# Kernel optimization log

Hardware: AMD Instinct MI355X
Metric: run time of the kernel (lower is better)

The kernel has to match this reference:

```python
import jax, jax.numpy as jnp
import numpy as np

B, C, H, W = 1, 96, 128, 128
P = 4            # patch_size
E = 192          # embed_dim
DI = 384         # d_inner = expand * embed_dim
NS = 16          # d_state
R = 12           # dt_rank = ceil(E/16)
K = 4            # scan directions
NBLK = 8         # SS2D_MBs_num
GW = C // 2      # SCPA group width


def layernorm(x, g, b, eps=1e-5):
    mu = x.mean(-1, keepdims=True)
    v = x.var(-1, keepdims=True)
    return (x - mu) * jax.lax.rsqrt(v + eps) * g + b


def batchnorm(x, g, b, m, v, eps=1e-5):
    # eval-mode BatchNorm2d over channel axis 1 of (B,C,H,W)
    return (x - m[:, None, None]) * jax.lax.rsqrt(v + eps)[:, None, None] * g[:, None, None] + b[:, None, None]


def conv2d(x, w):
    return jax.lax.conv_general_dilated(x, w, (1, 1), 'SAME', dimension_numbers=('NCHW', 'OIHW', 'NCHW'))


def dwconv2d(x, w, b):
    out = jax.lax.conv_general_dilated(x, w[:, None], (1, 1), 'SAME',
                                       dimension_numbers=('NCHW', 'OIHW', 'NCHW'),
                                       feature_group_count=w.shape[0])
    return out + b[None, :, None, None]


def lrelu(x):
    return jnp.where(x >= 0, x, 0.2 * x)


def channel_attention(x, w1, w2):
    # CBAM-style: shared MLP on avg+max pooled channel descriptors, sigmoid gate
    avg = x.mean((2, 3))
    mx = x.max((2, 3))
    mlp = lambda v: jax.nn.relu(v @ w1.T) @ w2.T
    attn = jax.nn.sigmoid(mlp(avg) + mlp(mx))
    return x * attn[:, :, None, None]


def selective_scan(xs, dts, A, Bs, Cs, Dskip):
    # xs,dts: (B,K,DI,L); A: (K,DI,NS); Bs,Cs: (B,K,NS,L); Dskip: (K,DI)
    xs_t = jnp.moveaxis(xs, -1, 0)
    dts_t = jnp.moveaxis(dts, -1, 0)
    Bs_t = jnp.moveaxis(Bs, -1, 0)
    Cs_t = jnp.moveaxis(Cs, -1, 0)
    h0 = jnp.zeros(xs.shape[:3] + (NS,), xs.dtype)  # (B,K,DI,NS)

    def step(h, t):
        xt, dt, Bt, Ct = t
        h = jnp.exp(dt[..., None] * A) * h + (dt * xt)[..., None] * Bt[:, :, None, :]
        return h, jnp.sum(h * Ct[:, :, None, :], axis=-1)

    _, ys = jax.lax.scan(step, h0, (xs_t, dts_t, Bs_t, Cs_t))
    return jnp.moveaxis(ys, 0, -1) + xs * Dskip[None, :, :, None]


def ss2d_block(x, p):
    # VMamba-style VSS block: x + SS2D(LN(x)); x: (B,Hp,Wp,E)
    (ln_g, ln_b, inproj_w, conv_w, conv_b, xproj_w, dtproj_w, dtproj_b,
     Alog, Dskip, on_g, on_b, outproj_w, merge_w) = p
    Bsz, Hp, Wp, _ = x.shape
    L = Hp * Wp
    h = layernorm(x, ln_g, ln_b)
    xz = jnp.einsum('bhwd,ed->bhwe', h, inproj_w)   # (B,Hp,Wp,2*DI)
    xc, z = jnp.split(xz, 2, axis=-1)
    xc = jax.nn.silu(dwconv2d(jnp.transpose(xc, (0, 3, 1, 2)), conv_w, conv_b))  # (B,DI,Hp,Wp)
    # 4-direction cross-scan: row-major, col-major and their reverses
    xf = xc.reshape(Bsz, DI, L)
    xwh = jnp.transpose(xc, (0, 1, 3, 2)).reshape(Bsz, DI, L)
    xs = jnp.stack([xf, xwh, jnp.flip(xf, -1), jnp.flip(xwh, -1)], axis=1)  # (B,K,DI,L)
    x_dbl = jnp.einsum('bkdl,kcd->bkcl', xs, xproj_w)  # (B,K,R+2*NS,L)
    dts, Bm, Cm = jnp.split(x_dbl, [R, R + NS], axis=2)
    dts = jax.nn.softplus(jnp.einsum('bkrl,kdr->bkdl', dts, dtproj_w) + dtproj_b[None, :, :, None])
    A = -jnp.exp(Alog)
    oy = selective_scan(xs, dts, A, Bm, Cm, Dskip)  # (B,K,DI,L)
    y0 = oy[:, 0]
    y1 = jnp.transpose(oy[:, 1].reshape(Bsz, DI, Wp, Hp), (0, 1, 3, 2)).reshape(Bsz, DI, L)
    y2 = jnp.flip(oy[:, 2], -1)
    y3 = jnp.transpose(jnp.flip(oy[:, 3], -1).reshape(Bsz, DI, Wp, Hp), (0, 1, 3, 2)).reshape(Bsz, DI, L)
    y = merge_w[0] * y0 + merge_w[1] * y1 + merge_w[2] * y2 + merge_w[3] * y3  # learnable merge
    y = jnp.transpose(y, (0, 2, 1)).reshape(Bsz, Hp, Wp, DI)
    y = layernorm(y, on_g, on_b) * jax.nn.silu(z)
    return x + jnp.einsum('bhwd,ed->bhwe', y, outproj_w)


def scpa(x, c1a, c1b, k1, k2w, k2b, k3, k4, c3):
    # PAN SCPA: two branches (3x3 conv / pixel-attention conv), 1x1 fuse, residual
    a = lrelu(jnp.einsum('bchw,oc->bohw', x, c1a))
    b = lrelu(jnp.einsum('bchw,oc->bohw', x, c1b))
    a = conv2d(a, k1)
    g = jax.nn.sigmoid(jnp.einsum('bchw,oc->bohw', b, k2w) + k2b[None, :, None, None])
    b = conv2d(conv2d(b, k3) * g, k4)
    out = jnp.einsum('bchw,oc->bohw', jnp.concatenate([lrelu(a), lrelu(b)], 1), c3)
    return out + x


def _forward(x, bn1_g, bn1_b, bn1_m, bn1_v, ca_w1, ca_w2, pe_w, pe_b, pu_w, pu_b,
             blk_ln_g, blk_ln_b, blk_inproj_w, blk_conv_w, blk_conv_b, blk_xproj_w,
             blk_dtproj_w, blk_dtproj_b, blk_Alog, blk_D, blk_on_g, blk_on_b,
             blk_outproj_w, blk_merge_w, bn2_g, bn2_b, bn2_m, bn2_v,
             scpa_c1a_w, scpa_c1b_w, scpa_k1_w, pa_k2_w, pa_k2_b, pa_k3_w, pa_k4_w, scpa_c3_w):
    residual = x
    h = batchnorm(x, bn1_g, bn1_b, bn1_m, bn1_v)
    x1 = channel_attention(h, ca_w1, ca_w2)
    Hp, Wp = H // P, W // P
    # patch embed: (B,C,H,W) -> (B,Hp,Wp,C*P*P) -> linear -> (B,Hp,Wp,E)
    xp = h.reshape(B, C, Hp, P, Wp, P).transpose(0, 2, 4, 1, 3, 5).reshape(B, Hp, Wp, C * P * P)
    x2 = xp @ pe_w.T + pe_b
    blk_params = (blk_ln_g, blk_ln_b, blk_inproj_w, blk_conv_w, blk_conv_b, blk_xproj_w,
                  blk_dtproj_w, blk_dtproj_b, blk_Alog, blk_D, blk_on_g, blk_on_b,
                  blk_outproj_w, blk_merge_w)
    x2, _ = jax.lax.scan(lambda c, p: (ss2d_block(c, p), None), x2, blk_params)
    # patch unembed
    xu = x2 @ pu_w.T + pu_b
    xu = xu.reshape(B, Hp, Wp, C, P, P).transpose(0, 3, 1, 4, 2, 5).reshape(B, C, H, W)
    xsum = residual + x1 + xu
    h2 = batchnorm(xsum, bn2_g, bn2_b, bn2_m, bn2_v)
    out = scpa(h2, scpa_c1a_w, scpa_c1b_w, scpa_k1_w, pa_k2_w, pa_k2_b, pa_k3_w, pa_k4_w, scpa_c3_w)
    return out + xsum


def setup_inputs():
    key = jax.random.key(0)
    kct = [0]
    def nk():
        kct[0] += 1
        return jax.random.fold_in(key, kct[0])
    def nrm(shape, s=0.02):
        return (jax.random.normal(nk(), shape) * s).astype(jnp.float32)
    f32 = jnp.float32
    inp = dict(
        x=jax.random.normal(nk(), (B, C, H, W), dtype=f32),
        bn1_g=jnp.ones((C,), f32), bn1_b=jnp.zeros((C,), f32),
        bn1_m=nrm((C,), 0.05), bn1_v=jnp.ones((C,), f32),
        ca_w1=nrm((C // 16, C), 0.1), ca_w2=nrm((C, C // 16), 0.1),
        pe_w=nrm((E, C * P * P)), pe_b=jnp.zeros((E,), f32),
        pu_w=nrm((C * P * P, E)), pu_b=jnp.zeros((C * P * P,), f32),
        blk_ln_g=jnp.ones((NBLK, E), f32), blk_ln_b=jnp.zeros((NBLK, E), f32),
        blk_inproj_w=nrm((NBLK, 2 * DI, E)),
        blk_conv_w=nrm((NBLK, DI, 3, 3), 0.1),
        blk_conv_b=jnp.zeros((NBLK, DI), f32),
        blk_xproj_w=nrm((NBLK, K, R + 2 * NS, DI)),
        blk_dtproj_w=nrm((NBLK, K, DI, R), 0.1),
        blk_dtproj_b=jnp.full((NBLK, K, DI), -4.6, f32),  # softplus ~= 0.01
        blk_Alog=jnp.broadcast_to(jnp.log(jnp.arange(1, NS + 1, dtype=f32)), (NBLK, K, DI, NS)) + 0.0,
        blk_D=jnp.ones((NBLK, K, DI), f32),
        blk_on_g=jnp.ones((NBLK, DI), f32), blk_on_b=jnp.zeros((NBLK, DI), f32),
        blk_outproj_w=nrm((NBLK, E, DI)),
        blk_merge_w=jnp.ones((NBLK, K), f32),
        bn2_g=jnp.ones((C,), f32), bn2_b=jnp.zeros((C,), f32),
        bn2_m=nrm((C,), 0.05), bn2_v=jnp.ones((C,), f32),
        scpa_c1a_w=nrm((GW, C), 0.05), scpa_c1b_w=nrm((GW, C), 0.05),
        scpa_k1_w=nrm((GW, GW, 3, 3), 0.05),
        pa_k2_w=nrm((GW, GW), 0.05), pa_k2_b=jnp.zeros((GW,), f32),
        pa_k3_w=nrm((GW, GW, 3, 3), 0.05), pa_k4_w=nrm((GW, GW, 3, 3), 0.05),
        scpa_c3_w=nrm((C, 2 * GW), 0.05),
    )
    return inp


def reference(x, bn1_g, bn1_b, bn1_m, bn1_v, ca_w1, ca_w2, pe_w, pe_b, pu_w, pu_b,
              blk_ln_g, blk_ln_b, blk_inproj_w, blk_conv_w, blk_conv_b, blk_xproj_w,
              blk_dtproj_w, blk_dtproj_b, blk_Alog, blk_D, blk_on_g, blk_on_b,
              blk_outproj_w, blk_merge_w, bn2_g, bn2_b, bn2_m, bn2_v,
              scpa_c1a_w, scpa_c1b_w, scpa_k1_w, pa_k2_w, pa_k2_b, pa_k3_w, pa_k4_w, scpa_c3_w):
    return _forward(x, bn1_g, bn1_b, bn1_m, bn1_v, ca_w1, ca_w2, pe_w, pe_b, pu_w, pu_b,
                    blk_ln_g, blk_ln_b, blk_inproj_w, blk_conv_w, blk_conv_b, blk_xproj_w,
                    blk_dtproj_w, blk_dtproj_b, blk_Alog, blk_D, blk_on_g, blk_on_b,
                    blk_outproj_w, blk_merge_w, bn2_g, bn2_b, bn2_m, bn2_v,
                    scpa_c1a_w, scpa_c1b_w, scpa_k1_w, pa_k2_w, pa_k2_b, pa_k3_w, pa_k4_w, scpa_c3_w)
```

## Files before the change

kernel.cpp:

```cpp
#include <hip/hip_runtime.h>
#include <math.h>

#define HW 16384
constexpr int C_ = 96;
constexpr int E_ = 192, DI_ = 384, NS_ = 16, R_ = 12, K_ = 4, NBLK_ = 8, GW_ = 48;
constexpr int L_ = 1024, CXP_ = 44;
constexpr int TC_ = 64;
constexpr int NCH_ = L_ / TC_;

__device__ __forceinline__ float lrelu_(float x){ return x >= 0.f ? x : 0.2f*x; }
__device__ __forceinline__ float sigmoid_(float x){ return 1.f/(1.f+expf(-x)); }
__device__ __forceinline__ float silu_(float x){ return x/(1.f+expf(-x)); }
__device__ __forceinline__ float softplus_(float x){ return fmaxf(x,0.f)+log1pf(expf(-fabsf(x))); }

__global__ void k_transpose(const float* __restrict__ in, float* __restrict__ out,
                            int rows, int cols, int in_stride){
  __shared__ float t[32][33];
  const float* ib = in + (size_t)blockIdx.z*rows*in_stride;
  float* ob = out + (size_t)blockIdx.z*rows*cols;
  int r0 = blockIdx.y*32, c0 = blockIdx.x*32;
  int tx = threadIdx.x, ty = threadIdx.y;
  for (int i=0;i<32;i+=8){
    int r = r0+ty+i, c = c0+tx;
    if (r<rows && c<cols) t[ty+i][tx] = ib[(size_t)r*in_stride+c];
  }
  __syncthreads();
  for (int i=0;i<32;i+=8){
    int c = c0+ty+i, r = r0+tx;
    if (r<rows && c<cols) ob[(size_t)c*rows+r] = t[tx][ty+i];
  }
}

__global__ void k_bn1(const float* __restrict__ x, const float* g, const float* b,
                      const float* m, const float* v,
                      float* __restrict__ h, float* __restrict__ stats,
                      float* __restrict__ su, float* __restrict__ sq){
  int c = blockIdx.x, tid = threadIdx.x;
  int gid = c*256 + tid;
  if (gid < 1024){ su[gid] = 0.f; sq[gid] = 0.f; }
  float sc = g[c]*rsqrtf(v[c]+1e-5f), sh = b[c]-m[c]*sc;
  const float* xc = x + (size_t)c*HW;
  float* hc = h + (size_t)c*HW;
  float s = 0.f, mx = -1e30f;
  for (int i=tid;i<HW;i+=256){
    float val = fmaf(xc[i], sc, sh);
    hc[i] = val; s += val; mx = fmaxf(mx, val);
  }
  for (int o=32;o;o>>=1){ s += __shfl_xor(s,o); mx = fmaxf(mx, __shfl_xor(mx,o)); }
  __shared__ float ss[4], sm[4];
  int wid = tid>>6, lane = tid&63;
  if (!lane){ ss[wid]=s; sm[wid]=mx; }
  __syncthreads();
  if (!tid){
    stats[c] = (ss[0]+ss[1]+ss[2]+ss[3])*(1.f/HW);
    stats[96+c] = fmaxf(fmaxf(sm[0],sm[1]),fmaxf(sm[2],sm[3]));
  }
}

__global__ void k_attn(const float* __restrict__ stats, const float* __restrict__ w1,
                       const float* __restrict__ w2, float* __restrict__ attn){
  __shared__ float hid[12];
  int tid = threadIdx.x;
  if (tid < 12){
    int j = tid%6, which = tid/6;
    const float* vv = stats + which*96;
    float a = 0.f;
    for (int c=0;c<96;c++) a += vv[c]*w1[j*96+c];
    hid[tid] = fmaxf(a, 0.f);
  }
  __syncthreads();
  if (tid < 96){
    float a = 0.f;
    for (int j=0;j<6;j++) a += (hid[j]+hid[6+j])*w2[tid*6+j];
    attn[tid] = sigmoid_(a);
  }
}

__global__ __launch_bounds__(256) void k_gemmPE(const float* __restrict__ hsrc,
                      const float* __restrict__ wt, const float* __restrict__ bias,
                      float* __restrict__ out, float* __restrict__ su, float* __restrict__ sq){
  const int K = 1536, N = 192;
  __shared__ float As[32][34];
  __shared__ float Bs[32][32];
  int tid = threadIdx.x;
  int m0 = blockIdx.x*32, n0 = blockIdx.y*32;
  int tx = tid&15, ty = tid>>4;
  int arow = tid>>3, akq = tid&7;
  int brow = tid>>3, bn4 = tid&7;
  int m = m0+arow;
  int base2 = (m>>5)*512 + (m&31)*4;
  auto aload = [&](int kk)->float4 {
    int c = kk>>4, i2 = (kk>>2)&3;
    return *(const float4*)&hsrc[((size_t)c<<14) + (size_t)(i2*128 + base2)];
  };
  float4 aR = aload(akq*4);
  float4 bR = *(const float4*)&wt[(size_t)brow*N + n0 + bn4*4];
  float acc[2][2] = {{0}};
  for (int k0=0; k0<K; k0+=32){
    __syncthreads();
    As[akq*4+0][arow]=aR.x; As[akq*4+1][arow]=aR.y;
    As[akq*4+2][arow]=aR.z; As[akq*4+3][arow]=aR.w;
    *(float4*)&Bs[brow][bn4*4] = bR;
    __syncthreads();
    if (k0+32 < K){
      aR = aload(k0+32+akq*4);
      bR = *(const float4*)&wt[(size_t)(k0+32+brow)*N + n0 + bn4*4];
    }
    #pragma unroll
    for (int kk=0; kk<32; kk++){
      float2 av = *(const float2*)&As[kk][ty*2];
      float2 bv = *(const float2*)&Bs[kk][tx*2];
      acc[0][0] = fmaf(av.x, bv.x, acc[0][0]);
      acc[0][1] = fmaf(av.x, bv.y, acc[0][1]);
      acc[1][0] = fmaf(av.y, bv.x, acc[1][0]);
      acc[1][1] = fmaf(av.y, bv.y, acc[1][1]);
    }
  }
  float2 bq = *(const float2*)&bias[n0+tx*2];
  float sl[2], ql[2];
  #pragma unroll
  for (int i=0;i<2;i++){
    size_t o = (size_t)(m0+ty*2+i)*N + n0 + tx*2;
    float2 ov; ov.x = acc[i][0]+bq.x; ov.y = acc[i][1]+bq.y;
    *(float2*)&out[o] = ov;
    sl[i] = ov.x+ov.y; ql[i] = ov.x*ov.x+ov.y*ov.y;
  }
  #pragma unroll
  for (int o=8;o;o>>=1){
    sl[0]+=__shfl_xor(sl[0],o); ql[0]+=__shfl_xor(ql[0],o);
    sl[1]+=__shfl_xor(sl[1],o); ql[1]+=__shfl_xor(ql[1],o);
  }
  if (tx==0){
    atomicAdd(&su[m0+ty*2],   sl[0]); atomicAdd(&sq[m0+ty*2],   ql[0]);
    atomicAdd(&su[m0+ty*2+1], sl[1]); atomicAdd(&sq[m0+ty*2+1], ql[1]);
  }
}

__global__ __launch_bounds__(256) void k_gemm32s(const float* __restrict__ act,
                      const float* __restrict__ wt, const float* __restrict__ res,
                      float* __restrict__ out, float* __restrict__ su, float* __restrict__ sq,
                      int K, int N){
  __shared__ float As[32][34];
  __shared__ float Bs[32][32];
  int tid = threadIdx.x;
  int m0 = blockIdx.x*32, n0 = blockIdx.y*32;
  int tx = tid&15, ty = tid>>4;
  int arow = tid>>3, akq = tid&7;
  int brow = tid>>3, bn4 = tid&7;
  float4 aR = *(const float4*)&act[(size_t)(m0+arow)*K + akq*4];
  float4 bR = *(const float4*)&wt [(size_t)brow*N + n0 + bn4*4];
  float acc[2][2] = {{0}};
  for (int k0=0; k0<K; k0+=32){
    __syncthreads();
    As[akq*4+0][arow]=aR.x; As[akq*4+1][arow]=aR.y;
    As[akq*4+2][arow]=aR.z; As[akq*4+3][arow]=aR.w;
    *(float4*)&Bs[brow][bn4*4] = bR;
    __syncthreads();
    if (k0+32 < K){
      aR = *(const float4*)&act[(size_t)(m0+arow)*K + k0+32 + akq*4];
      bR = *(const float4*)&wt [(size_t)(k0+32+brow)*N + n0 + bn4*4];
    }
    #pragma unroll
    for (int kk=0; kk<32; kk++){
      float2 av = *(const float2*)&As[kk][ty*2];
      float2 bv = *(const float2*)&Bs[kk][tx*2];
      acc[0][0] = fmaf(av.x, bv.x, acc[0][0]);
      acc[0][1] = fmaf(av.x, bv.y, acc[0][1]);
      acc[1][0] = fmaf(av.y, bv.x, acc[1][0]);
      acc[1][1] = fmaf(av.y, bv.y, acc[1][1]);
    }
  }
  float sl[2], ql[2];
  #pragma unroll
  for (int i=0;i<2;i++){
    size_t o = (size_t)(m0+ty*2+i)*N + n0 + tx*2;
    float2 r = *(const float2*)&res[o];
    float2 ov; ov.x = acc[i][0]+r.x; ov.y = acc[i][1]+r.y;
    *(float2*)&out[o] = ov;
    sl[i] = ov.x+ov.y; ql[i] = ov.x*ov.x+ov.y*ov.y;
  }
  #pragma unroll
  for (int o=8;o;o>>=1){
// ... 33 lines not shown
    #pragma unroll
    for (int kk=0; kk<32; kk++){
      float2 av = *(const float2*)&As[kk][ty*2];
      float2 bv = *(const float2*)&Bs[kk][tx*2];
      acc[0][0] = fmaf(av.x, bv.x, acc[0][0]);
      acc[0][1] = fmaf(av.x, bv.y, acc[0][1]);
      acc[1][0] = fmaf(av.y, bv.x, acc[1][0]);
      acc[1][1] = fmaf(av.y, bv.y, acc[1][1]);
    }
  }
  int n = n0 + tx*2;
  float2 bq = *(const float2*)&bias[n];
  int c = n>>4, i2 = (n>>2)&3, j = n&3;
  #pragma unroll
  for (int i=0;i<2;i++){
    int m = m0+ty*2+i;
    size_t o = ((size_t)c<<14) + (size_t)((m>>5)*4+i2)*128 + (m&31)*4 + j;
    float2 ov; ov.x = acc[i][0]+bq.x; ov.y = acc[i][1]+bq.y;
    *(float2*)&out[o] = ov;
  }
}

__global__ __launch_bounds__(256) void k_gemm32ln(const float* __restrict__ act,
                      const float* __restrict__ wt, const float* __restrict__ lg,
                      const float* __restrict__ lb, const float* __restrict__ su,
                      const float* __restrict__ sq, float* __restrict__ out,
                      int K, int N){
  __shared__ float As[32][34];
  __shared__ float Bs[32][32];
  int tid = threadIdx.x;
  int m0 = blockIdx.x*32, n0 = blockIdx.y*32;
  int tx = tid&15, ty = tid>>4;
  int arow = tid>>3, akq = tid&7;
  int brow = tid>>3, bn4 = tid&7;
  float m = su[m0+arow]*(1.f/192.f);
  float r = rsqrtf(sq[m0+arow]*(1.f/192.f) - m*m + 1e-5f);
  float4 aR = *(const float4*)&act[(size_t)(m0+arow)*K + akq*4];
  float4 gR = *(const float4*)&lg[akq*4];
  float4 hR = *(const float4*)&lb[akq*4];
  float4 bR = *(const float4*)&wt[(size_t)brow*N + n0 + bn4*4];
  float acc[2][2] = {{0}};
  for (int k0=0; k0<K; k0+=32){
    __syncthreads();
    As[akq*4+0][arow] = (aR.x-m)*r*gR.x + hR.x;
    As[akq*4+1][arow] = (aR.y-m)*r*gR.y + hR.y;
    As[akq*4+2][arow] = (aR.z-m)*r*gR.z + hR.z;
    As[akq*4+3][arow] = (aR.w-m)*r*gR.w + hR.w;
    *(float4*)&Bs[brow][bn4*4] = bR;
    __syncthreads();
    if (k0+32 < K){
      aR = *(const float4*)&act[(size_t)(m0+arow)*K + k0+32 + akq*4];
      gR = *(const float4*)&lg[k0+32+akq*4];
      hR = *(const float4*)&lb[k0+32+akq*4];
      bR = *(const float4*)&wt[(size_t)(k0+32+brow)*N + n0 + bn4*4];
    }
    #pragma unroll
    for (int kk=0; kk<32; kk++){
      float2 av = *(const float2*)&As[kk][ty*2];
      float2 bv = *(const float2*)&Bs[kk][tx*2];
      acc[0][0] = fmaf(av.x, bv.x, acc[0][0]);
      acc[0][1] = fmaf(av.x, bv.y, acc[0][1]);
      acc[1][0] = fmaf(av.y, bv.x, acc[1][0]);
      acc[1][1] = fmaf(av.y, bv.y, acc[1][1]);
    }
  }
  #pragma unroll
  for (int i=0;i<2;i++){
    size_t o = (size_t)(m0+ty*2+i)*N + n0 + tx*2;
    float2 ov; ov.x = acc[i][0]; ov.y = acc[i][1];
    *(float2*)&out[o] = ov;
  }
}

__global__ __launch_bounds__(256) void k_dwxst(const float* __restrict__ xz,
                        const float* __restrict__ w, const float* __restrict__ bias,
                        float* __restrict__ xcs, float* __restrict__ xst0,
                        float* __restrict__ xst1){
  __shared__ float ld[96][33];
  __shared__ float t[32][33];
  int h0 = blockIdx.x;
  int d0 = blockIdx.y*32;
  int tx = threadIdx.x, ty = threadIdx.y;
  #pragma unroll
  for (int i=0;i<12;i++){
    int ll = i*8 + ty;
    int h = h0 - 1 + (ll>>5);
    int wv = ll & 31;
    float v = 0.f;
    if ((unsigned)h < 32u) v = xz[(size_t)(h*32+wv)*768 + d0 + tx];
    ld[ll][tx] = v;
  }
  __syncthreads();
  #pragma unroll
  for (int i=0;i<4;i++){
    int dl = ty + 8*i;
    int d = d0 + dl;
    float acc = bias[d];
    const float* wp = w + d*9;
    #pragma unroll
    for (int di=0;di<3;di++){
      #pragma unroll
      for (int dj=0;dj<3;dj++){
        int wq = tx + dj - 1;
        if ((unsigned)wq < 32u)
          acc = fmaf(ld[di*32 + wq][dl], wp[di*3+dj], acc);
      }
    }
    float val = silu_(acc);
    xcs[(size_t)d*L_ + h0*32 + tx] = val;
    t[dl][tx] = val;
  }
  __syncthreads();
  int d = d0 + tx;
  #pragma unroll
  for (int i=0;i<4;i++){
    int wq = ty + 8*i;
    int l = h0*32 + wq;
    float val = t[tx][wq];
    int t1 = wq*32 + h0;
    xst0[(size_t)l*DI_ + d] = val;
    xst1[(size_t)t1*DI_ + d] = val;
  }
}

__global__ __launch_bounds__(256) void k_xdblP(const float* __restrict__ xcs,
                       const float* __restrict__ xw, float* __restrict__ xdblP){
  int kz = blockIdx.z;
  int k = kz & 3, sp = kz >> 2;
  int s = blockIdx.x*256 + threadIdx.x;
  int Ts = ((s&31)<<5) | (s>>5);
  int lw;
  if (k==0) lw = s;
  else if (k==1) lw = Ts;
  else if (k==2) lw = 1023-s;
  else lw = 1023-Ts;
  int c0 = blockIdx.y*4;
  const float* wp = xw + ((size_t)k*CXP_ + c0)*DI_ + sp*128;
  const float* src = xcs + s + (size_t)sp*128*L_;
  float a0=0,a1=0,a2=0,a3=0;
  for (int d=0; d<128; d++){
    float v = src[(size_t)d*L_];
    a0 = fmaf(v, wp[d],        a0);
    a1 = fmaf(v, wp[DI_+d],    a1);
    a2 = fmaf(v, wp[2*DI_+d],  a2);
    a3 = fmaf(v, wp[3*DI_+d],  a3);
  }
  size_t base = (((size_t)sp*4 + k)*CXP_ + c0)*L_ + lw;
  xdblP[base]       = a0;
  xdblP[base+L_]    = a1;
  xdblP[base+2*L_]  = a2;
  xdblP[base+3*L_]  = a3;
}

__global__ void k_dtbc(const float* __restrict__ xdblP, const float* __restrict__ dtw,
                       const float* __restrict__ dtb, float* __restrict__ dts_t,
                       float* __restrict__ bc){
  int k = blockIdx.y, l = blockIdx.x, d = threadIdx.x;
  const float* p0 = xdblP + ((size_t)(0+k)*CXP_)*L_ + l;
  const float* p1 = xdblP + ((size_t)(4+k)*CXP_)*L_ + l;
  const float* p2 = xdblP + ((size_t)(8+k)*CXP_)*L_ + l;
  float acc = dtb[(size_t)k*DI_ + d];
  const float* w = dtw + ((size_t)k*DI_ + d)*R_;
  #pragma unroll
  for (int r=0;r<R_;r++){
    size_t o = (size_t)r*L_;
    acc = fmaf(p0[o]+p1[o]+p2[o], w[r], acc);
  }
  dts_t[((size_t)k*L_ + l)*DI_ + d] = softplus_(acc);
  if (d < 32){
    size_t o = (size_t)(R_+d)*L_;
    bc[((size_t)k*L_ + l)*32 + d] = p0[o]+p1[o]+p2[o];
  }
}

__global__ __launch_bounds__(256) void k_scanA(const float* __restrict__ xst0,
                      const float* __restrict__ xst1,
                      const float* __restrict__ dts_t, const float* __restrict__ bc,
                      const float* __restrict__ Alog,
                      float* __restrict__ Ech, float* __restrict__ Hch){
  int k = blockIdx.z;
  int d = blockIdx.y*16 + (threadIdx.x>>4);
  int n = threadIdx.x&15;
  int ch = blockIdx.x;
  float A = -expf(Alog[((size_t)k*DI_ + d)*NS_ + n]);
  float aL2 = A * 1.4426950408889634f;
  int t0 = ch*TC_;
  const float* dtp = dts_t + ((size_t)k*L_ + t0)*DI_ + d;
  const float* bcp = bc    + ((size_t)k*L_ + t0)*32;
  const float* xb = (k&1) ? xst1 : xst0;
  const float* xp_; ptrdiff_t xs_;
  if (k < 2){ xp_ = xb + (size_t)t0*DI_ + d; xs_ = DI_; }
  else      { xp_ = xb + (size_t)(1023-t0)*DI_ + d; xs_ = -(ptrdiff_t)DI_; }
  float h = 0.f, Ep = 1.f;
  #pragma unroll 4
  for (int t=0;t<TC_;t++){
    float dt = dtp[(size_t)t*DI_];
    float xv = xp_[(ptrdiff_t)t*xs_];
    float Bn = bcp[t*32+n];
    float e = exp2f(aL2*dt);
    h = fmaf(e, h, dt*xv*Bn);
    Ep *= e;
  }
  size_t idx = (((size_t)k*NCH_ + ch)*DI_ + d)*NS_ + n;
  Ech[idx] = Ep; Hch[idx] = h;
}

__global__ void k_scanB(const float* __restrict__ Ech, const float* __restrict__ Hch,
                        float* __restrict__ carry){
  int idx = blockIdx.x*256 + threadIdx.x;
  int k = idx / (DI_*NS_);
  int dn = idx % (DI_*NS_);
  float h = 0.f;
  #pragma unroll
  for (int c=0;c<NCH_;c++){
    size_t o = ((size_t)(k*NCH_+c)*DI_*NS_) + dn;
    carry[o] = h;
    h = fmaf(Ech[o], h, Hch[o]);
  }
}

__global__ __launch_bounds__(256) void k_scanC(const float* __restrict__ xst0,
                      const float* __restrict__ xst1,
                      const float* __restrict__ dts_t, const float* __restrict__ bc,
                      const float* __restrict__ Alog, const float* __restrict__ carry,
                      float* __restrict__ yst){
  int k = blockIdx.z;
  int d = blockIdx.y*16 + (threadIdx.x>>4);
  int n = threadIdx.x&15;
  int ch = blockIdx.x;
  float A = -expf(Alog[((size_t)k*DI_ + d)*NS_ + n]);
  float aL2 = A * 1.4426950408889634f;
  int t0 = ch*TC_;
  const float* dtp = dts_t + ((size_t)k*L_ + t0)*DI_ + d;
  const float* bcp = bc    + ((size_t)k*L_ + t0)*32;
  const float* xb = (k&1) ? xst1 : xst0;
  const float* xp_; ptrdiff_t xs_;
  if (k < 2){ xp_ = xb + (size_t)t0*DI_ + d; xs_ = DI_; }
  else      { xp_ = xb + (size_t)(1023-t0)*DI_ + d; xs_ = -(ptrdiff_t)DI_; }
  float* yp = yst + ((size_t)k*L_ + t0)*DI_ + d;
  float h = carry[(((size_t)k*NCH_ + ch)*DI_ + d)*NS_ + n];
  #pragma unroll 4
  for (int t=0;t<TC_;t++){
    float dt = dtp[(size_t)t*DI_];
    float xv = xp_[(ptrdiff_t)t*xs_];
    float Bn = bcp[t*32+n], Cn = bcp[t*32+16+n];
    float e = exp2f(aL2*dt);
    h = fmaf(e, h, dt*xv*Bn);
    float p = h*Cn;
    p += __shfl_xor(p,1); p += __shfl_xor(p,2);
    p += __shfl_xor(p,4); p += __shfl_xor(p,8);
    if (n==0) yp[(size_t)t*DI_] = p;
  }
}

__global__ void k_merge(const float* __restrict__ yst, const float* __restrict__ xst0,
                        const float* __restrict__ xst1,
                        const float* __restrict__ Dsk, const float* __restrict__ mw,
                        const float* __restrict__ ong, const float* __restrict__ onb,
                        const float* __restrict__ xz, float* __restrict__ out,
                        float* __restrict__ su, float* __restrict__ sq){
  int l = blockIdx.x, d = threadIdx.x;
  if (d == 0){ su[l] = 0.f; sq[l] = 0.f; }
  int T = ((l&31)<<5) | (l>>5);
  int tt[4] = { l, T, 1023-l, 1023-T };
  float xv0 = xst0[(size_t)l*DI_ + d];
  float xv1 = xst1[(size_t)T*DI_ + d];
  float v = 0.f;
  #pragma unroll
  for (int k=0;k<4;k++){
    float xk = (k&1) ? xv1 : xv0;
    v += mw[k]*(yst[(size_t)(k*L_ + tt[k])*DI_ + d] + xk*Dsk[k*DI_+d]);
  }
  float s = v, sqv = v*v;
  for (int o=32;o;o>>=1){ s += __shfl_xor(s,o); sqv += __shfl_xor(sqv,o); }
  __shared__ float rs_[6], rq_[6];
  int lane = d&63, wid = d>>6;
  if (!lane){ rs_[wid]=s; rq_[wid]=sqv; }
  __syncthreads();
  float ts=0.f, tq=0.f;
  #pragma unroll
  for (int i=0;i<6;i++){ ts += rs_[i]; tq += rq_[i]; }
  float mu = ts*(1.f/DI_);
  float rstd = rsqrtf(tq*(1.f/DI_) - mu*mu + 1e-5f);
  float y = (v-mu)*rstd*ong[d] + onb[d];
  float z = xz[(size_t)l*768 + DI_ + d];
  out[(size_t)l*DI_ + d] = y * silu_(z);
}

__global__ void k_sum(const float* __restrict__ x, const float* __restrict__ h,
                      const float* __restrict__ attn, const float* __restrict__ xu,
                      const float* g2, const float* b2, const float* m2, const float* v2,
                      float* __restrict__ xsum, float* __restrict__ h2){
  int idx = blockIdx.x*256 + threadIdx.x;
  int c = idx>>14;
  float s = x[idx] + h[idx]*attn[c] + xu[idx];
  xsum[idx] = s;
  h2[idx] = (s - m2[c])*rsqrtf(v2[c]+1e-5f)*g2[c] + b2[c];
}

__global__ __launch_bounds__(256) void k_1x1ab(const float* __restrict__ h2,
                        const float* __restrict__ wa, const float* __restrict__ wb,
                        float* __restrict__ a, float* __restrict__ b){
  __shared__ float lw[96*12];
  int ocg = blockIdx.x;
  for (int i=threadIdx.x; i<96*12; i+=256){
    int o = i%12, c = i/12;
    lw[i] = (o<6) ? wa[(ocg*6 + o)*96 + c] : wb[(ocg*6 + (o-6))*96 + c];
  }
  __syncthreads();
  int p = blockIdx.y*256 + threadIdx.x;
  float acc[12];
  #pragma unroll
  for (int o=0;o<12;o++) acc[o]=0.f;
  for (int c=0;c<96;c++){
    float v = h2[(size_t)c*HW + p];
    const float* w = lw + c*12;
    #pragma unroll
    for (int o=0;o<12;o++) acc[o] = fmaf(v, w[o], acc[o]);
  }
  #pragma unroll
  for (int o=0;o<6;o++){
    a[(size_t)(ocg*6+o)*HW + p] = lrelu_(acc[o]);
    b[(size_t)(ocg*6+o)*HW + p] = lrelu_(acc[6+o]);
  }
}

__global__ __launch_bounds__(256) void k_1x1g(const float* __restrict__ b,
                       const float* __restrict__ w, const float* __restrict__ bias,
                       float* __restrict__ g){
  __shared__ float lw[48*6];
  int ocg = blockIdx.x;
  for (int i=threadIdx.x; i<48*6; i+=256){
    int o = i%6, c = i/6;
    lw[i] = w[(ocg*6 + o)*48 + c];
  }
  __syncthreads();
  int p = blockIdx.y*256 + threadIdx.x;
  float acc[6];
  #pragma unroll
  for (int o=0;o<6;o++) acc[o] = bias[ocg*6+o];
  for (int c=0;c<48;c++){
    float v = b[(size_t)c*HW + p];
    const float* wp = lw + c*6;
    #pragma unroll
    for (int o=0;o<6;o++) acc[o] = fmaf(v, wp[o], acc[o]);
  }
  #pragma unroll
  for (int o=0;o<6;o++) g[(size_t)(ocg*6+o)*HW + p] = sigmoid_(acc[o]);
}

__global__ __launch_bounds__(256) void k_conv3d(const float* __restrict__ inA,
                        const float* __restrict__ wA, const float* __restrict__ inB,
                        const float* __restrict__ wB, const float* __restrict__ aux,
                        float* __restrict__ outA, float* __restrict__ outB){
  __shared__ float lw[48*9*6];
  int half = blockIdx.x >> 3;
  int ocg = blockIdx.x & 7;
  const float* in = half ? inB : inA;
  const float* w  = half ? wB : wA;
  for (int i=threadIdx.x; i<48*9*6; i+=256){
    int o = i%6, j = (i/6)%9, ic = i/54;
    lw[i] = w[((size_t)(ocg*6+o)*48 + ic)*9 + j];
  }
  __syncthreads();
  int p = blockIdx.y*256 + threadIdx.x;
  int hh = p>>7, ww = p&127;
  float acc[6];
  #pragma unroll
  for (int o=0;o<6;o++) acc[o]=0.f;
  for (int ic=0; ic<48; ic++){
    const float* ip = in + (size_t)ic*HW;
    float xv[9];
    #pragma unroll
    for (int di=0;di<3;di++){
      int y = hh+di-1;
      bool yok = (unsigned)y < 128u;
      #pragma unroll
      for (int dj=0;dj<3;dj++){
        int xx = ww+dj-1;
        bool ok = yok && ((unsigned)xx < 128u);
        xv[di*3+dj] = ok ? ip[y*128+xx] : 0.f;
      }
    }
    const float* lwp = lw + ic*54;
    #pragma unroll
    for (int j=0;j<9;j++){
      float xj = xv[j];
      const float* wj = lwp + j*6;
      #pragma unroll
      for (int o=0;o<6;o++) acc[o] = fmaf(xj, wj[o], acc[o]);
    }
  }
  if (half == 0){
    #pragma unroll
    for (int o=0;o<6;o++)
      outA[(size_t)(ocg*6+o)*HW + p] = lrelu_(acc[o]);
  } else {
    #pragma unroll
    for (int o=0;o<6;o++){
      size_t oi = (size_t)(ocg*6+o)*HW + p;
      outB[oi] = acc[o]*aux[oi];
    }
  }
}

__global__ __launch_bounds__(256) void k_conv3(const float* __restrict__ in,
                        const float* __restrict__ w, float* __restrict__ out){
  __shared__ float lw[48*9*6];
  int ocg = blockIdx.x;
  for (int i=threadIdx.x; i<48*9*6; i+=256){
    int o = i%6, j = (i/6)%9, ic = i/54;
    lw[i] = w[((size_t)(ocg*6+o)*48 + ic)*9 + j];
  }
  __syncthreads();
  int p = blockIdx.y*256 + threadIdx.x;
  int hh = p>>7, ww = p&127;
  float acc[6];
  #pragma unroll
  for (int o=0;o<6;o++) acc[o]=0.f;
  for (int ic=0; ic<48; ic++){
    const float* ip = in + (size_t)ic*HW;
    float xv[9];
    #pragma unroll
    for (int di=0;di<3;di++){
      int y = hh+di-1;
      bool yok = (unsigned)y < 128u;
      #pragma unroll
      for (int dj=0;dj<3;dj++){
        int xx = ww+dj-1;
        bool ok = yok && ((unsigned)xx < 128u);
        xv[di*3+dj] = ok ? ip[y*128+xx] : 0.f;
      }
    }
    const float* lwp = lw + ic*54;
    #pragma unroll
    for (int j=0;j<9;j++){
      float xj = xv[j];
      const float* wj = lwp + j*6;
      #pragma unroll
      for (int o=0;o<6;o++) acc[o] = fmaf(xj, wj[o], acc[o]);
    }
  }
  #pragma unroll
  for (int o=0;o<6;o++)
    out[(size_t)(ocg*6+o)*HW + p] = lrelu_(acc[o]);
}

__global__ __launch_bounds__(256) void k_c3(const float* __restrict__ ab,
                     const float* __restrict__ w, const float* __restrict__ h2,
                     const float* __restrict__ xsum, float* __restrict__ out){
  __shared__ float lw[96*12];
  int ocg = blockIdx.x;
  for (int i=threadIdx.x; i<96*12; i+=256){
    int o = i%12, j = i/12;
    lw[i] = w[(ocg*12 + o)*96 + j];
  }
  __syncthreads();
  int p = blockIdx.y*256 + threadIdx.x;
  float acc[12];
  #pragma unroll
  for (int o=0;o<12;o++) acc[o]=0.f;
  for (int j=0;j<96;j++){
    float v = ab[(size_t)j*HW + p];
    const float* wp = lw + j*12;
    #pragma unroll
    for (int o=0;o<12;o++) acc[o] = fmaf(v, wp[o], acc[o]);
  }
  #pragma unroll
  for (int o=0;o<12;o++){
    size_t oi = (size_t)(ocg*12+o)*HW + p;
    out[oi] = acc[o] + h2[oi] + xsum[oi];
  }
}

extern "C" void kernel_launch(void* const* d_in, const int* in_sizes, int n_in,
                              void* d_out, int out_size, void* d_ws, size_t ws_size,
                              hipStream_t stream){
  (void)in_sizes; (void)n_in; (void)out_size; (void)ws_size;
  const float* x    = (const float*)d_in[0];
  const float* bn1g = (const float*)d_in[1];
  const float* bn1b = (const float*)d_in[2];
  const float* bn1m = (const float*)d_in[3];
  const float* bn1v = (const float*)d_in[4];
  const float* caw1 = (const float*)d_in[5];
  const float* caw2 = (const float*)d_in[6];
  const float* peW  = (const float*)d_in[7];
  const float* peb  = (const float*)d_in[8];
  const float* puW  = (const float*)d_in[9];
  const float* pub  = (const float*)d_in[10];
  const float* lng  = (const float*)d_in[11];
  const float* lnb  = (const float*)d_in[12];
  const float* inW  = (const float*)d_in[13];
  const float* convw= (const float*)d_in[14];
  const float* convb= (const float*)d_in[15];
  const float* xprojw=(const float*)d_in[16];
  const float* dtw  = (const float*)d_in[17];
  const float* dtb  = (const float*)d_in[18];
  const float* Alog = (const float*)d_in[19];
  const float* Dsk  = (const float*)d_in[20];
  const float* ong  = (const float*)d_in[21];
  const float* onb  = (const float*)d_in[22];
  const float* outW = (const float*)d_in[23];
  const float* mw   = (const float*)d_in[24];
  const float* bn2g = (const float*)d_in[25];
  const float* bn2b = (const float*)d_in[26];
  const float* bn2m = (const float*)d_in[27];
  const float* bn2v = (const float*)d_in[28];
  const float* c1a  = (const float*)d_in[29];
  const float* c1b  = (const float*)d_in[30];
  const float* k1w  = (const float*)d_in[31];
  const float* k2w  = (const float*)d_in[32];
  const float* k2b  = (const float*)d_in[33];
  const float* k3w  = (const float*)d_in[34];
  const float* k4w  = (const float*)d_in[35];
  const float* c3w  = (const float*)d_in[36];
  float* out = (float*)d_out;

  float* ws = (float*)d_ws;
  size_t off = 0;
  auto alloc = [&](size_t n){ float* p = ws + off; off += n; return p; };
  float* peWT  = alloc((size_t)1536*192);
  float* puWT  = alloc((size_t)192*1536);
  float* inWT  = alloc((size_t)8*192*768);
  float* outWT = alloc((size_t)8*384*192);
  float* bufH  = alloc((size_t)96*HW);
  float* stats = alloc(256);
  float* attn  = alloc(128);
  float* bufP  = alloc((size_t)1024*1536);
  float* x2a   = alloc((size_t)1024*192);
  float* x2b   = alloc((size_t)1024*192);
  float* bufXZ = alloc((size_t)1024*768);
  float* bufXCS= alloc((size_t)384*1024);
  float* bufXST= alloc((size_t)4*1024*384);
  float* xdblP = alloc((size_t)12*44*1024);
  float* dts   = alloc((size_t)4*1024*384);
  float* bc    = alloc((size_t)4*1024*32);
  float* yst   = alloc((size_t)4*1024*384);
  float* bufY  = alloc((size_t)1024*384);
  float* xsum  = alloc((size_t)96*HW);
  float* h2    = alloc((size_t)96*HW);
  float* Ech   = alloc((size_t)K_*NCH_*DI_*NS_);
  float* Hch   = alloc((size_t)K_*NCH_*DI_*NS_);
  float* carry = alloc((size_t)K_*NCH_*DI_*NS_);
  float* suB   = alloc(1024);
  float* sqB   = alloc(1024);
  float* xst0  = bufXST;
  float* xst1  = bufXST + (size_t)L_*DI_;

  dim3 tb(32,8);
  k_transpose<<<dim3(48,6,1), tb, 0, stream>>>(peW, peWT, 192, 1536, 1536);
  k_transpose<<<dim3(6,48,1), tb, 0, stream>>>(puW, puWT, 1536, 192, 192);
  k_transpose<<<dim3(6,24,8), tb, 0, stream>>>(inW, inWT, 768, 192, 192);
  k_transpose<<<dim3(12,6,8), tb, 0, stream>>>(outW, outWT, 192, 384, 384);

  k_bn1<<<96,256,0,stream>>>(x, bn1g, bn1b, bn1m, bn1v, bufH, stats, suB, sqB);
  k_attn<<<1,128,0,stream>>>(stats, caw1, caw2, attn);
  k_gemmPE<<<dim3(32,6),256,0,stream>>>(bufH, peWT, peb, x2a, suB, sqB);

  float* cur = x2a; float* nxt = x2b;
  for (int b=0;b<8;b++){
    k_gemm32ln<<<dim3(32,24),256,0,stream>>>(cur, inWT+(size_t)b*192*768,
                        lng+(size_t)b*192, lnb+(size_t)b*192, suB, sqB, bufXZ, 192, 768);
    k_dwxst<<<dim3(32,12),tb,0,stream>>>(bufXZ, convw+(size_t)b*384*9,
                        convb+(size_t)b*384, bufXCS, xst0, xst1);
    k_xdblP<<<dim3(4,11,12),256,0,stream>>>(bufXCS, xprojw+(size_t)b*4*44*384, xdblP);
    k_dtbc<<<dim3(1024,4),384,0,stream>>>(xdblP, dtw+(size_t)b*4*384*12, dtb+(size_t)b*4*384, dts, bc);
    const float* Ab = Alog + (size_t)b*4*384*16;
    k_scanA<<<dim3(NCH_,DI_/16,4),256,0,stream>>>(xst0, xst1, dts, bc, Ab, Ech, Hch);
    k_scanB<<<(K_*DI_*NS_)/256,256,0,stream>>>(Ech, Hch, carry);
    k_scanC<<<dim3(NCH_,DI_/16,4),256,0,stream>>>(xst0, xst1, dts, bc, Ab, carry, yst);
    k_merge<<<1024,384,0,stream>>>(yst, xst0, xst1, Dsk+(size_t)b*4*384, mw+(size_t)b*4,
                                   ong+(size_t)b*384, onb+(size_t)b*384, bufXZ, bufY, suB, sqB);
    k_gemm32s<<<dim3(32,6),256,0,stream>>>(bufY, outWT+(size_t)b*384*192, cur, nxt, suB, sqB, 384, 192);
    float* t = cur; cur = nxt; nxt = t;
  }

  k_gemmPU<<<dim3(32,48),256,0,stream>>>(cur, puWT, pub, bufP);
  k_sum<<<(96*HW)/256,256,0,stream>>>(x, bufH, attn, bufP, bn2g, bn2b, bn2m, bn2v, xsum, h2);

  float* bufA = dts;
  float* bufB = dts + (size_t)48*HW;
  float* bufG = yst;
  float* bufT = yst + (size_t)48*HW;
  float* ab   = bufXST;
  k_1x1ab<<<dim3(8,64),256,0,stream>>>(h2, c1a, c1b, bufA, bufB);
  k_1x1g<<<dim3(8,64),256,0,stream>>>(bufB, k2w, k2b, bufG);
  k_conv3d<<<dim3(16,64),256,0,stream>>>(bufA, k1w, bufB, k3w, bufG, ab, bufT);
  k_conv3<<<dim3(8,64),256,0,stream>>>(bufT, k4w, ab+(size_t)48*HW);
  k_c3<<<dim3(8,64),256,0,stream>>>(ab, c3w, h2, xsum, out);
}
```

Baseline: 1.125 ms.

## Fuse dt projection and B/C reduction into scan kernels; merge weight transposes

Removes the separate k_dtbc kernel. Each scan chunk block now sums the three xdblP partials into shared memory and computes softplus(dt) for its 16 channels and 64 timesteps on the fly. This is done in both the scanA and scanC passes, so the dt projection work is duplicated, but the dts/bc global round trip and one launch per block are gone. The four weight-transpose launches are also combined into a single launch.

```diff
diff --git a/kernel.cpp b/kernel.cpp
--- a/kernel.cpp
+++ b/kernel.cpp
@@ -13,21 +13,28 @@
 __device__ __forceinline__ float silu_(float x){ return x/(1.f+expf(-x)); }
 __device__ __forceinline__ float softplus_(float x){ return fmaxf(x,0.f)+log1pf(expf(-fabsf(x))); }
 
-__global__ void k_transpose(const float* __restrict__ in, float* __restrict__ out,
-                            int rows, int cols, int in_stride){
+__global__ void k_transAll(const float* __restrict__ peW, float* __restrict__ peWT,
+                           const float* __restrict__ puW, float* __restrict__ puWT,
+                           const float* __restrict__ inW, float* __restrict__ inWT,
+                           const float* __restrict__ outW, float* __restrict__ outWT){
   __shared__ float t[32][33];
-  const float* ib = in + (size_t)blockIdx.z*rows*in_stride;
-  float* ob = out + (size_t)blockIdx.z*rows*cols;
-  int r0 = blockIdx.y*32, c0 = blockIdx.x*32;
-  int tx = threadIdx.x, ty = threadIdx.y;
+  int id = blockIdx.x;
+  const float* in; float* out; int rows, cols, bx, by;
+  if (id < 288){ in=peW; out=peWT; rows=192; cols=1536; bx=id%48; by=id/48; }
+  else if (id < 576){ int r=id-288; in=puW; out=puWT; rows=1536; cols=192; bx=r%6; by=r/6; }
+  else if (id < 1728){ int r=id-576; int z=r/144; int q=r%144;
+    in=inW+(size_t)z*768*192; out=inWT+(size_t)z*768*192; rows=768; cols=192; bx=q%6; by=q/6; }
+  else { int r=id-1728; int z=r/72; int q=r%72;
+    in=outW+(size_t)z*192*384; out=outWT+(size_t)z*192*384; rows=192; cols=384; bx=q%12; by=q/12; }
+  int r0=by*32, c0=bx*32, tx=threadIdx.x, ty=threadIdx.y;
   for (int i=0;i<32;i+=8){
-    int r = r0+ty+i, c = c0+tx;
-    if (r<rows && c<cols) t[ty+i][tx] = ib[(size_t)r*in_stride+c];
+    int r=r0+ty+i, c=c0+tx;
+    if (r<rows && c<cols) t[ty+i][tx]=in[(size_t)r*cols+c];
   }
   __syncthreads();
   for (int i=0;i<32;i+=8){
-    int c = c0+ty+i, r = r0+tx;
-    if (r<rows && c<cols) ob[(size_t)c*rows+r] = t[tx][ty+i];
+    int c=c0+ty+i, r=r0+tx;
+    if (r<rows && c<cols) out[(size_t)c*rows+r]=t[tx][ty+i];
   }
 }
 
@@ -367,41 +374,40 @@
   xdblP[base+3*L_]  = a3;
 }
 
-__global__ void k_dtbc(const float* __restrict__ xdblP, const float* __restrict__ dtw,
-                       const float* __restrict__ dtb, float* __restrict__ dts_t,
-                       float* __restrict__ bc){
-  int k = blockIdx.y, l = blockIdx.x, d = threadIdx.x;
-  const float* p0 = xdblP + ((size_t)(0+k)*CXP_)*L_ + l;
-  const float* p1 = xdblP + ((size_t)(4+k)*CXP_)*L_ + l;
-  const float* p2 = xdblP + ((size_t)(8+k)*CXP_)*L_ + l;
-  float acc = dtb[(size_t)k*DI_ + d];
-  const float* w = dtw + ((size_t)k*DI_ + d)*R_;
-  #pragma unroll
-  for (int r=0;r<R_;r++){
-    size_t o = (size_t)r*L_;
-    acc = fmaf(p0[o]+p1[o]+p2[o], w[r], acc);
-  }
-  dts_t[((size_t)k*L_ + l)*DI_ + d] = softplus_(acc);
-  if (d < 32){
-    size_t o = (size_t)(R_+d)*L_;
-    bc[((size_t)k*L_ + l)*32 + d] = p0[o]+p1[o]+p2[o];
-  }
-}
-
-__global__ __launch_bounds__(256) void k_scanA(const float* __restrict__ xst0,
-                      const float* __restrict__ xst1,
-                      const float* __restrict__ dts_t, const float* __restrict__ bc,
+__global__ __launch_bounds__(256) void k_scanAF(const float* __restrict__ xst0,
+                      const float* __restrict__ xst1, const float* __restrict__ xdblP,
+                      const float* __restrict__ dtw, const float* __restrict__ dtb,
                       const float* __restrict__ Alog,
                       float* __restrict__ Ech, float* __restrict__ Hch){
-  int k = blockIdx.z;
-  int d = blockIdx.y*16 + (threadIdx.x>>4);
-  int n = threadIdx.x&15;
-  int ch = blockIdx.x;
+  __shared__ float ps[44][65];
+  __shared__ float dl[64][17];
+  int k = blockIdx.z, dg = blockIdx.y, ch = blockIdx.x;
+  int t0 = ch*TC_;
+  int tid = threadIdx.x;
+  for (int i = tid; i < 44*64; i += 256){
+    int c = i>>6, l = i&63;
+    size_t o = ((size_t)k*CXP_ + c)*L_ + t0 + l;
+    ps[c][l] = xdblP[o] + xdblP[o + (size_t)4*CXP_*L_] + xdblP[o + (size_t)8*CXP_*L_];
+  }
+  __syncthreads();
+  int d0 = dg*16;
+  {
+    int l = tid & 63;
+    for (int dli = tid>>6; dli < 16; dli += 4){
+      int d = d0 + dli;
+      float acc = dtb[(size_t)k*DI_ + d];
+      const float* w = dtw + ((size_t)k*DI_ + d)*R_;
+      #pragma unroll
+      for (int r=0;r<R_;r++) acc = fmaf(ps[r][l], w[r], acc);
+      dl[l][dli] = softplus_(acc);
+    }
+  }
+  __syncthreads();
+  int d = d0 + (tid>>4);
+  int n = tid&15;
+  int dli = tid>>4;
   float A = -expf(Alog[((size_t)k*DI_ + d)*NS_ + n]);
   float aL2 = A * 1.4426950408889634f;
-  int t0 = ch*TC_;
-  const float* dtp = dts_t + ((size_t)k*L_ + t0)*DI_ + d;
-  const float* bcp = bc    + ((size_t)k*L_ + t0)*32;
   const float* xb = (k&1) ? xst1 : xst0;
   const float* xp_; ptrdiff_t xs_;
   if (k < 2){ xp_ = xb + (size_t)t0*DI_ + d; xs_ = DI_; }
@@ -409,9 +415,9 @@
   float h = 0.f, Ep = 1.f;
   #pragma unroll 4
   for (int t=0;t<TC_;t++){
-    float dt = dtp[(size_t)t*DI_];
+    float dt = dl[t][dli];
     float xv = xp_[(ptrdiff_t)t*xs_];
-    float Bn = bcp[t*32+n];
+    float Bn = ps[R_+n][t];
     float e = exp2f(aL2*dt);
     h = fmaf(e, h, dt*xv*Bn);
     Ep *= e;
@@ -434,20 +440,40 @@
   }
 }
 
-__global__ __launch_bounds__(256) void k_scanC(const float* __restrict__ xst0,
-                      const float* __restrict__ xst1,
-                      const float* __restrict__ dts_t, const float* __restrict__ bc,
+__global__ __launch_bounds__(256) void k_scanCF(const float* __restrict__ xst0,
+                      const float* __restrict__ xst1, const float* __restrict__ xdblP,
+                      const float* __restrict__ dtw, const float* __restrict__ dtb,
                       const float* __restrict__ Alog, const float* __restrict__ carry,
                       float* __restrict__ yst){
-  int k = blockIdx.z;
-  int d = blockIdx.y*16 + (threadIdx.x>>4);
-  int n = threadIdx.x&15;
-  int ch = blockIdx.x;
+  __shared__ float ps[44][65];
+  __shared__ float dl[64][17];
+  int k = blockIdx.z, dg = blockIdx.y, ch = blockIdx.x;
+  int t0 = ch*TC_;
+  int tid = threadIdx.x;
+  for (int i = tid; i < 44*64; i += 256){
+    int c = i>>6, l = i&63;
+    size_t o = ((size_t)k*CXP_ + c)*L_ + t0 + l;
+    ps[c][l] = xdblP[o] + xdblP[o + (size_t)4*CXP_*L_] + xdblP[o + (size_t)8*CXP_*L_];
+  }
+  __syncthreads();
+  int d0 = dg*16;
+  {
+    int l = tid & 63;
+    for (int dli = tid>>6; dli < 16; dli += 4){
+      int d = d0 + dli;
+      float acc = dtb[(size_t)k*DI_ + d];
+      const float* w = dtw + ((size_t)k*DI_ + d)*R_;
+      #pragma unroll
+      for (int r=0;r<R_;r++) acc = fmaf(ps[r][l], w[r], acc);
+      dl[l][dli] = softplus_(acc);
+    }
+  }
+  __syncthreads();
+  int d = d0 + (tid>>4);
+  int n = tid&15;
+  int dli = tid>>4;
   float A = -expf(Alog[((size_t)k*DI_ + d)*NS_ + n]);
   float aL2 = A * 1.4426950408889634f;
-  int t0 = ch*TC_;
-  const float* dtp = dts_t + ((size_t)k*L_ + t0)*DI_ + d;
-  const float* bcp = bc    + ((size_t)k*L_ + t0)*32;
   const float* xb = (k&1) ? xst1 : xst0;
   const float* xp_; ptrdiff_t xs_;
   if (k < 2){ xp_ = xb + (size_t)t0*DI_ + d; xs_ = DI_; }
@@ -456,9 +482,9 @@
   float h = carry[(((size_t)k*NCH_ + ch)*DI_ + d)*NS_ + n];
   #pragma unroll 4
   for (int t=0;t<TC_;t++){
-    float dt = dtp[(size_t)t*DI_];
+    float dt = dl[t][dli];
     float xv = xp_[(ptrdiff_t)t*xs_];
-    float Bn = bcp[t*32+n], Cn = bcp[t*32+16+n];
+    float Bn = ps[R_+n][t], Cn = ps[R_+16+n][t];
     float e = exp2f(aL2*dt);
     h = fmaf(e, h, dt*xv*Bn);
     float p = h*Cn;
@@ -749,7 +775,6 @@
   float* bufXST= alloc((size_t)4*1024*384);
   float* xdblP = alloc((size_t)12*44*1024);
   float* dts   = alloc((size_t)4*1024*384);
-  float* bc    = alloc((size_t)4*1024*32);
   float* yst   = alloc((size_t)4*1024*384);
   float* bufY  = alloc((size_t)1024*384);
   float* xsum  = alloc((size_t)96*HW);
@@ -763,10 +788,7 @@
   float* xst1  = bufXST + (size_t)L_*DI_;
 
   dim3 tb(32,8);
-  k_transpose<<<dim3(48,6,1), tb, 0, stream>>>(peW, peWT, 192, 1536, 1536);
-  k_transpose<<<dim3(6,48,1), tb, 0, stream>>>(puW, puWT, 1536, 192, 192);
-  k_transpose<<<dim3(6,24,8), tb, 0, stream>>>(inW, inWT, 768, 192, 192);
-  k_transpose<<<dim3(12,6,8), tb, 0, stream>>>(outW, outWT, 192, 384, 384);
+  k_transAll<<<2304, tb, 0, stream>>>(peW, peWT, puW, puWT, inW, inWT, outW, outWT);
 
   k_bn1<<<96,256,0,stream>>>(x, bn1g, bn1b, bn1m, bn1v, bufH, stats, suB, sqB);
   k_attn<<<1,128,0,stream>>>(stats, caw1, caw2, attn);
@@ -779,11 +801,12 @@
     k_dwxst<<<dim3(32,12),tb,0,stream>>>(bufXZ, convw+(size_t)b*384*9,
                         convb+(size_t)b*384, bufXCS, xst0, xst1);
     k_xdblP<<<dim3(4,11,12),256,0,stream>>>(bufXCS, xprojw+(size_t)b*4*44*384, xdblP);
-    k_dtbc<<<dim3(1024,4),384,0,stream>>>(xdblP, dtw+(size_t)b*4*384*12, dtb+(size_t)b*4*384, dts, bc);
     const float* Ab = Alog + (size_t)b*4*384*16;
-    k_scanA<<<dim3(NCH_,DI_/16,4),256,0,stream>>>(xst0, xst1, dts, bc, Ab, Ech, Hch);
+    const float* dwb = dtw + (size_t)b*4*384*12;
+    const float* dbb = dtb + (size_t)b*4*384;
+    k_scanAF<<<dim3(NCH_,24,4),256,0,stream>>>(xst0, xst1, xdblP, dwb, dbb, Ab, Ech, Hch);
     k_scanB<<<(K_*DI_*NS_)/256,256,0,stream>>>(Ech, Hch, carry);
-    k_scanC<<<dim3(NCH_,DI_/16,4),256,0,stream>>>(xst0, xst1, dts, bc, Ab, carry, yst);
+    k_scanCF<<<dim3(NCH_,24,4),256,0,stream>>>(xst0, xst1, xdblP, dwb, dbb, Ab, carry, yst);
     k_merge<<<1024,384,0,stream>>>(yst, xst0, xst1, Dsk+(size_t)b*4*384, mw+(size_t)b*4,
                                    ong+(size_t)b*384, onb+(size_t)b*384, bufXZ, bufY, suB, sqB);
     k_gemm32s<<<dim3(32,6),256,0,stream>>>(bufY, outWT+(size_t)b*384*192, cur, nxt, suB, sqB, 384, 192);
```

Result: slower. 1.148 ms (+2.0%).

## Stage conv input rows in shared memory and merge weight transposes into one launch

Applied to the files above, without the earlier changes.

The 3x3 convolution kernels now load an 8-channel slab of four padded image rows into LDS per iteration and read the 9-tap neighbourhood from there. This replaces the nine bounds-checked global loads per input channel per thread. The four weight-transpose launches are also combined into a single kernel that dispatches on block index, removing three launches. The conv change adds extra barriers and LDS traffic per channel group in exchange for less redundant global memory access.

```diff
diff --git a/kernel.cpp b/kernel.cpp
--- a/kernel.cpp
+++ b/kernel.cpp
@@ -13,21 +13,28 @@
 __device__ __forceinline__ float silu_(float x){ return x/(1.f+expf(-x)); }
 __device__ __forceinline__ float softplus_(float x){ return fmaxf(x,0.f)+log1pf(expf(-fabsf(x))); }
 
-__global__ void k_transpose(const float* __restrict__ in, float* __restrict__ out,
-                            int rows, int cols, int in_stride){
+__global__ void k_transAll(const float* __restrict__ peW, float* __restrict__ peWT,
+                           const float* __restrict__ puW, float* __restrict__ puWT,
+                           const float* __restrict__ inW, float* __restrict__ inWT,
+                           const float* __restrict__ outW, float* __restrict__ outWT){
   __shared__ float t[32][33];
-  const float* ib = in + (size_t)blockIdx.z*rows*in_stride;
-  float* ob = out + (size_t)blockIdx.z*rows*cols;
-  int r0 = blockIdx.y*32, c0 = blockIdx.x*32;
-  int tx = threadIdx.x, ty = threadIdx.y;
+  int id = blockIdx.x;
+  const float* in; float* out; int rows, cols, bx, by;
+  if (id < 288){ in=peW; out=peWT; rows=192; cols=1536; bx=id%48; by=id/48; }
+  else if (id < 576){ int r=id-288; in=puW; out=puWT; rows=1536; cols=192; bx=r%6; by=r/6; }
+  else if (id < 1728){ int r=id-576; int z=r/144; int q=r%144;
+    in=inW+(size_t)z*768*192; out=inWT+(size_t)z*768*192; rows=768; cols=192; bx=q%6; by=q/6; }
+  else { int r=id-1728; int z=r/72; int q=r%72;
+    in=outW+(size_t)z*192*384; out=outWT+(size_t)z*192*384; rows=192; cols=384; bx=q%12; by=q/12; }
+  int r0=by*32, c0=bx*32, tx=threadIdx.x, ty=threadIdx.y;
   for (int i=0;i<32;i+=8){
-    int r = r0+ty+i, c = c0+tx;
-    if (r<rows && c<cols) t[ty+i][tx] = ib[(size_t)r*in_stride+c];
+    int r=r0+ty+i, c=c0+tx;
+    if (r<rows && c<cols) t[ty+i][tx]=in[(size_t)r*cols+c];
   }
   __syncthreads();
   for (int i=0;i<32;i+=8){
-    int c = c0+ty+i, r = r0+tx;
-    if (r<rows && c<cols) ob[(size_t)c*rows+r] = t[tx][ty+i];
+    int c=c0+ty+i, r=r0+tx;
+    if (r<rows && c<cols) out[(size_t)c*rows+r]=t[tx][ty+i];
   }
 }
 
@@ -569,41 +576,48 @@
                         const float* __restrict__ wB, const float* __restrict__ aux,
                         float* __restrict__ outA, float* __restrict__ outB){
   __shared__ float lw[48*9*6];
+  __shared__ float ld[8][4][130];
   int half = blockIdx.x >> 3;
   int ocg = blockIdx.x & 7;
   const float* in = half ? inB : inA;
   const float* w  = half ? wB : wA;
-  for (int i=threadIdx.x; i<48*9*6; i+=256){
+  int tid = threadIdx.x;
+  for (int i=tid; i<48*9*6; i+=256){
     int o = i%6, j = (i/6)%9, ic = i/54;
     lw[i] = w[((size_t)(ocg*6+o)*48 + ic)*9 + j];
   }
-  __syncthreads();
-  int p = blockIdx.y*256 + threadIdx.x;
-  int hh = p>>7, ww = p&127;
+  if (tid < 32){ ld[tid>>2][tid&3][0] = 0.f; ld[tid>>2][tid&3][129] = 0.f; }
+  int p = blockIdx.y*256 + tid;
+  int ww = p&127;
+  int hbase = blockIdx.y*2 - 1;
+  int lr = 1 + (tid>>7);
   float acc[6];
   #pragma unroll
   for (int o=0;o<6;o++) acc[o]=0.f;
-  for (int ic=0; ic<48; ic++){
-    const float* ip = in + (size_t)ic*HW;
-    float xv[9];
-    #pragma unroll
-    for (int di=0;di<3;di++){
-      int y = hh+di-1;
-      bool yok = (unsigned)y < 128u;
+  for (int ic0=0; ic0<48; ic0+=8){
+    __syncthreads();
+    #pragma unroll
+    for (int q=0;q<16;q++){
+      int i = tid + q*256;
+      int icl = i>>9, rem = i&511;
+      int r = rem>>7, cp = rem&127;
+      int gy = hbase + r;
+      ld[icl][r][cp+1] = ((unsigned)gy < 128u) ? in[(size_t)(ic0+icl)*HW + gy*128 + cp] : 0.f;
+    }
+    __syncthreads();
+    #pragma unroll
+    for (int icl=0; icl<8; icl++){
+      const float* lwp = lw + (ic0+icl)*54;
       #pragma unroll
-      for (int dj=0;dj<3;dj++){
-        int xx = ww+dj-1;
-        bool ok = yok && ((unsigned)xx < 128u);
-        xv[di*3+dj] = ok ? ip[y*128+xx] : 0.f;
+      for (int di=0;di<3;di++){
+        #pragma unroll
+        for (int dj=0;dj<3;dj++){
+          float xv = ld[icl][lr-1+di][ww+dj];
+          const float* wj = lwp + (di*3+dj)*6;
+          #pragma unroll
+          for (int o=0;o<6;o++) acc[o] = fmaf(xv, wj[o], acc[o]);
+        }
       }
-    }
-    const float* lwp = lw + ic*54;
-    #pragma unroll
-    for (int j=0;j<9;j++){
-      float xj = xv[j];
-      const float* wj = lwp + j*6;
-      #pragma unroll
-      for (int o=0;o<6;o++) acc[o] = fmaf(xj, wj[o], acc[o]);
     }
   }
   if (half == 0){
@@ -622,38 +636,45 @@
 __global__ __launch_bounds__(256) void k_conv3(const float* __restrict__ in,
                         const float* __restrict__ w, float* __restrict__ out){
   __shared__ float lw[48*9*6];
+  __shared__ float ld[8][4][130];
   int ocg = blockIdx.x;
-  for (int i=threadIdx.x; i<48*9*6; i+=256){
+  int tid = threadIdx.x;
+  for (int i=tid; i<48*9*6; i+=256){
     int o = i%6, j = (i/6)%9, ic = i/54;
     lw[i] = w[((size_t)(ocg*6+o)*48 + ic)*9 + j];
   }
-  __syncthreads();
-  int p = blockIdx.y*256 + threadIdx.x;
-  int hh = p>>7, ww = p&127;
+  if (tid < 32){ ld[tid>>2][tid&3][0] = 0.f; ld[tid>>2][tid&3][129] = 0.f; }
+  int p = blockIdx.y*256 + tid;
+  int ww = p&127;
+  int hbase = blockIdx.y*2 - 1;
+  int lr = 1 + (tid>>7);
   float acc[6];
   #pragma unroll
   for (int o=0;o<6;o++) acc[o]=0.f;
-  for (int ic=0; ic<48; ic++){
-    const float* ip = in + (size_t)ic*HW;
-    float xv[9];
-    #pragma unroll
-    for (int di=0;di<3;di++){
-      int y = hh+di-1;
-      bool yok = (unsigned)y < 128u;
+  for (int ic0=0; ic0<48; ic0+=8){
+    __syncthreads();
+    #pragma unroll
+    for (int q=0;q<16;q++){
+      int i = tid + q*256;
+      int icl = i>>9, rem = i&511;
+      int r = rem>>7, cp = rem&127;
+      int gy = hbase + r;
+      ld[icl][r][cp+1] = ((unsigned)gy < 128u) ? in[(size_t)(ic0+icl)*HW + gy*128 + cp] : 0.f;
+    }
+    __syncthreads();
+    #pragma unroll
+    for (int icl=0; icl<8; icl++){
+      const float* lwp = lw + (ic0+icl)*54;
       #pragma unroll
-      for (int dj=0;dj<3;dj++){
-        int xx = ww+dj-1;
-        bool ok = yok && ((unsigned)xx < 128u);
-        xv[di*3+dj] = ok ? ip[y*128+xx] : 0.f;
+      for (int di=0;di<3;di++){
+        #pragma unroll
+        for (int dj=0;dj<3;dj++){
+          float xv = ld[icl][lr-1+di][ww+dj];
+          const float* wj = lwp + (di*3+dj)*6;
+          #pragma unroll
+          for (int o=0;o<6;o++) acc[o] = fmaf(xv, wj[o], acc[o]);
+        }
       }
-    }
-    const float* lwp = lw + ic*54;
-    #pragma unroll
-    for (int j=0;j<9;j++){
-      float xj = xv[j];
-      const float* wj = lwp + j*6;
-      #pragma unroll
-      for (int o=0;o<6;o++) acc[o] = fmaf(xj, wj[o], acc[o]);
     }
   }
   #pragma unroll
@@ -763,10 +784,7 @@
   float* xst1  = bufXST + (size_t)L_*DI_;
 
   dim3 tb(32,8);
-  k_transpose<<<dim3(48,6,1), tb, 0, stream>>>(peW, peWT, 192, 1536, 1536);
-  k_transpose<<<dim3(6,48,1), tb, 0, stream>>>(puW, puWT, 1536, 192, 192);
-  k_transpose<<<dim3(6,24,8), tb, 0, stream>>>(inW, inWT, 768, 192, 192);
-  k_transpose<<<dim3(12,6,8), tb, 0, stream>>>(outW, outWT, 192, 384, 384);
+  k_transAll<<<2304, tb, 0, stream>>>(peW, peWT, puW, puWT, inW, inWT, outW, outWT);
 
   k_bn1<<<96,256,0,stream>>>(x, bn1g, bn1b, bn1m, bn1v, bufH, stats, suB, sqB);
   k_attn<<<1,128,0,stream>>>(stats, caw1, caw2, attn);
```

Result: no change. 1.121 ms (-0.3%).
